# Performance work log

Hardware: AMD Instinct MI355X
Metric: run time of the kernel (lower is better)

The kernel has to match this reference:

```python
import jax, jax.numpy as jnp
import numpy as np

B, T, F, CI, CO, K, DIL = 16, 512, 32, 128, 128, 3, 2


def setup_inputs() -> dict:
    key = jax.random.key(0)
    k1, k2, k3 = jax.random.split(key, 3)
    x = jax.random.normal(k1, (B, T, F, CI), dtype=jnp.float32)
    # torch Conv1d weight per feature: [CO, CI, K]; stack over features -> [F, CO, CI, K]
    fan_in = CI * K
    bound = 1.0 / np.sqrt(fan_in)
    w = jax.random.uniform(k2, (F, CO, CI, K), dtype=jnp.float32, minval=-bound, maxval=bound)
    b = jax.random.uniform(k3, (F, CO), dtype=jnp.float32, minval=-bound, maxval=bound)
    return {"x": x, "w": w, "b": b}


def reference(x, w, b):
    # Causal dilated conv, independent filters per feature.
    left_pad = DIL * (K - 1)
    xpad = jnp.pad(x, ((0, 0), (left_pad, 0), (0, 0), (0, 0)))  # [B, T+L, F, CI]
    # taps[k] = xpad[:, k*DIL : k*DIL + T] -> stack over kernel taps: [K, B, T, F, CI]
    taps = jnp.stack([xpad[:, k * DIL:k * DIL + T] for k in range(K)], axis=0)
    # y[b,t,f,o] = sum_{k,i} taps[k,b,t,f,i] * w[f,o,i,k] + b[f,o]
    y = jnp.einsum('kbtfi,foik->btfo', taps, w) + b[None, None, :, :]
    return y  # dropout p=0.0 (eval) is identity
```

## Files before the change

kernel.cpp:

```cpp
#include <hip/hip_runtime.h>
#include <stdint.h>

#define B_ 16
#define T_ 512
#define F_ 32
#define CI_ 128
#define CO_ 128
#define K_ 3
#define LPAD 4
#define TM 64
#define XROWS (TM + LPAD)
#define XPITCH 136
#define WPITCH 32
#define CHUNK_ELEMS (CO_ * WPITCH)
#define NCHUNK 12
#define NXV 5

typedef __attribute__((ext_vector_type(8))) __bf16 bf16x8;
typedef __attribute__((ext_vector_type(4))) float f32x4;

__device__ __forceinline__ uint16_t f2bf(float x) {
  uint32_t u = __builtin_bit_cast(uint32_t, x);
  u += 0x7fffu + ((u >> 16) & 1u);
  return (uint16_t)(u >> 16);
}

__global__ __launch_bounds__(256) void repack_w(const float* __restrict__ w,
                                                uint16_t* __restrict__ wt2) {
  int idx = blockIdx.x * 256 + threadIdx.x;
  int i = idx & (CI_ - 1);
  int fo = idx >> 7;
  int o = fo & (CO_ - 1);
  int f = fo >> 7;
  const float* src = w + (size_t)idx * K_;
  float a0 = src[0], a1 = src[1], a2 = src[2];
  size_t base = ((size_t)f * NCHUNK + (i >> 5)) * CHUNK_ELEMS + o * WPITCH + (i & 31);
  wt2[base] = f2bf(a0);
  wt2[base + 4 * (size_t)CHUNK_ELEMS] = f2bf(a1);
  wt2[base + 8 * (size_t)CHUNK_ELEMS] = f2bf(a2);
}

template <bool PACKED>
__global__ __launch_bounds__(512, 4) void conv_main(
    const float* __restrict__ x, const uint16_t* __restrict__ wt2,
    const float* __restrict__ wraw, const float* __restrict__ bias,
    float* __restrict__ y) {
  __shared__ __align__(16) uint16_t xs[2][XROWS * XPITCH];

  const int bid = blockIdx.x;
  const int f = bid >> 4;
  const int b = bid & 15;

  const int tid = threadIdx.x;
  const int lane = tid & 63;
  const int wave = tid >> 6;
  const int l15 = lane & 15;
  const int quad = lane >> 4;
  const int co0 = wave * 16;

  bf16x8 wreg[NCHUNK];
  if constexpr (PACKED) {
    const uint16_t* wp = wt2 + (size_t)f * NCHUNK * CHUNK_ELEMS + (co0 + l15) * WPITCH + quad * 8;
#pragma unroll
    for (int c = 0; c < NCHUNK; ++c)
      wreg[c] = *(const bf16x8*)(wp + c * CHUNK_ELEMS);
  } else {
#pragma unroll
    for (int c = 0; c < NCHUNK; ++c) {
      int tap = c >> 2, i0 = (c & 3) * 32 + quad * 8;
      const float* ws = wraw + (((size_t)(f * CO_ + co0 + l15)) * CI_ + i0) * K_ + tap;
      union { bf16x8 v; uint16_t h[8]; } u;
#pragma unroll
      for (int j = 0; j < 8; ++j) u.h[j] = f2bf(ws[j * K_]);
      wreg[c] = u.v;
    }
  }
  const float4 bb = *(const float4*)(bias + f * CO_ + co0 + quad * 4);

  const float* xb = x + ((size_t)b * T_ * F_ + f) * CI_;
  float4 xr[NXV];

  auto load_x = [&](int t0) {
#pragma unroll
    for (int it = 0; it < NXV; ++it) {
      int idx = tid + it * 512;
      if (idx < XROWS * 32) {
        int row = idx >> 5, c4 = idx & 31;
        int t = t0 - LPAD + row;
        xr[it] = (t >= 0) ? *(const float4*)(xb + (size_t)t * (F_ * CI_) + c4 * 4)
                          : make_float4(0.f, 0.f, 0.f, 0.f);
      }
    }
  };
  auto store_x = [&](uint16_t* dst) {
#pragma unroll
    for (int it = 0; it < NXV; ++it) {
      int idx = tid + it * 512;
      if (idx < XROWS * 32) {
        int row = idx >> 5, c4 = idx & 31;
        uint2 pk;
        pk.x = (uint32_t)f2bf(xr[it].x) | ((uint32_t)f2bf(xr[it].y) << 16);
        pk.y = (uint32_t)f2bf(xr[it].z) | ((uint32_t)f2bf(xr[it].w) << 16);
        *(uint2*)&dst[row * XPITCH + c4 * 4] = pk;
      }
    }
  };

  load_x(0);
  store_x(xs[0]);
  load_x(TM);
  __syncthreads();

  const int abase = l15 * XPITCH + quad * 8;

#pragma unroll 1
  for (int j = 0; j < 8; ++j) {
    const int t0 = j * TM;
    const uint16_t* xbuf = xs[j & 1];

    f32x4 acc[4];
#pragma unroll
    for (int fm = 0; fm < 4; ++fm) acc[fm] = (f32x4){bb.x, bb.y, bb.z, bb.w};

#pragma unroll
    for (int c = 0; c < NCHUNK; ++c) {
      const int tap = c >> 2, ks = c & 3;
#pragma unroll
      for (int fm = 0; fm < 4; ++fm) {
        bf16x8 av = *(const bf16x8*)&xbuf[abase + (2 * tap + fm * 16) * XPITCH + ks * 32];
        acc[fm] = __builtin_amdgcn_mfma_f32_16x16x32_bf16(wreg[c], av, acc[fm], 0, 0, 0);
      }
    }

    float* yb = y + (((size_t)b * T_ + t0 + l15) * F_ + f) * CO_ + co0 + quad * 4;
#pragma unroll
    for (int fm = 0; fm < 4; ++fm) {
      *(float4*)(yb + (size_t)(fm * 16) * (F_ * CO_)) =
          make_float4(acc[fm][0], acc[fm][1], acc[fm][2], acc[fm][3]);
    }

    if (j < 7) {
      store_x(xs[(j + 1) & 1]);
      if (j < 6) load_x((j + 2) * TM);
      __syncthreads();
    }
  }
}

extern "C" void kernel_launch(void* const* d_in, const int* in_sizes, int n_in,
                              void* d_out, int out_size, void* d_ws, size_t ws_size,
                              hipStream_t stream) {
  const float* x = (const float*)d_in[0];
  const float* w = (const float*)d_in[1];
  const float* bias = (const float*)d_in[2];
  float* y = (float*)d_out;

  const size_t wt2_bytes = (size_t)F_ * NCHUNK * CHUNK_ELEMS * sizeof(uint16_t);
  const int main_blocks = F_ * B_;

  if (ws_size >= wt2_bytes) {
    uint16_t* wt2 = (uint16_t*)d_ws;
    const int total = F_ * CO_ * CI_;
    repack_w<<<total / 256, 256, 0, stream>>>(w, wt2);
    conv_main<true><<<main_blocks, 512, 0, stream>>>(x, wt2, w, bias, y);
  } else {
    conv_main<false><<<main_blocks, 512, 0, stream>>>(x, (const uint16_t*)nullptr, w, bias, y);
  }
}
```

Before: 266.4 us.

## Swizzle x LDS layout and overlap staging and output stores with MFMA

```diff
diff --git a/kernel.cpp b/kernel.cpp
--- a/kernel.cpp
+++ b/kernel.cpp
@@ -9,8 +9,9 @@
 #define K_ 3
 #define LPAD 4
 #define TM 64
+#define NT 8
 #define XROWS (TM + LPAD)
-#define XPITCH 136
+#define XPITCH 128
 #define WPITCH 32
 #define CHUNK_ELEMS (CO_ * WPITCH)
 #define NCHUNK 12
@@ -101,7 +102,8 @@
         uint2 pk;
         pk.x = (uint32_t)f2bf(xr[it].x) | ((uint32_t)f2bf(xr[it].y) << 16);
         pk.y = (uint32_t)f2bf(xr[it].z) | ((uint32_t)f2bf(xr[it].w) << 16);
-        *(uint2*)&dst[row * XPITCH + c4 * 4] = pk;
+        int e = row * XPITCH + ((((c4 >> 1) ^ (row & 7)) << 3) | ((c4 & 1) << 2));
+        *(uint2*)&dst[e] = pk;
       }
     }
   };
@@ -111,12 +113,26 @@
   load_x(TM);
   __syncthreads();
 
-  const int abase = l15 * XPITCH + quad * 8;
+  f32x4 accp[4];
 
 #pragma unroll 1
-  for (int j = 0; j < 8; ++j) {
+  for (int j = 0; j < NT; ++j) {
     const int t0 = j * TM;
     const uint16_t* xbuf = xs[j & 1];
+
+    if (j < NT - 1) {
+      store_x(xs[(j + 1) & 1]);
+      if (j < NT - 2) load_x(t0 + 2 * TM);
+    }
+
+    if (j > 0) {
+      const int tp = t0 - TM;
+      float* yb = y + (((size_t)b * T_ + tp + l15) * F_ + f) * CO_ + co0 + quad * 4;
+#pragma unroll
+      for (int fm = 0; fm < 4; ++fm)
+        *(float4*)(yb + (size_t)(fm * 16) * (F_ * CO_)) =
+            make_float4(accp[fm][0], accp[fm][1], accp[fm][2], accp[fm][3]);
+    }
 
     f32x4 acc[4];
 #pragma unroll
@@ -127,23 +143,25 @@
       const int tap = c >> 2, ks = c & 3;
 #pragma unroll
       for (int fm = 0; fm < 4; ++fm) {
-        bf16x8 av = *(const bf16x8*)&xbuf[abase + (2 * tap + fm * 16) * XPITCH + ks * 32];
+        const int row = l15 + 2 * tap;
+        const int e = (row + fm * 16) * XPITCH + (((ks * 4 + quad) ^ (row & 7)) << 3);
+        bf16x8 av = *(const bf16x8*)&xbuf[e];
         acc[fm] = __builtin_amdgcn_mfma_f32_16x16x32_bf16(wreg[c], av, acc[fm], 0, 0, 0);
       }
     }
+#pragma unroll
+    for (int fm = 0; fm < 4; ++fm) accp[fm] = acc[fm];
 
-    float* yb = y + (((size_t)b * T_ + t0 + l15) * F_ + f) * CO_ + co0 + quad * 4;
+    if (j < NT - 1) __syncthreads();
+  }
+
+  {
+    const int tp = (NT - 1) * TM;
+    float* yb = y + (((size_t)b * T_ + tp + l15) * F_ + f) * CO_ + co0 + quad * 4;
 #pragma unroll
-    for (int fm = 0; fm < 4; ++fm) {
+    for (int fm = 0; fm < 4; ++fm)
       *(float4*)(yb + (size_t)(fm * 16) * (F_ * CO_)) =
-          make_float4(acc[fm][0], acc[fm][1], acc[fm][2], acc[fm][3]);
-    }
-
-    if (j < 7) {
-      store_x(xs[(j + 1) & 1]);
-      if (j < 6) load_x((j + 2) * TM);
-      __syncthreads();
-    }
+          make_float4(accp[fm][0], accp[fm][1], accp[fm][2], accp[fm][3]);
   }
 }
 
```

New measurement: 278.6 us. +4.6%, slower.
